# Kernel tuning notes

Measured on AMD Instinct MI355X. Metric: run time of the kernel, lower is better.

## Reference

```python
import jax, jax.numpy as jnp
import numpy as np
import math

N_HEAD = 16

def setup_inputs() -> dict:
    key = jax.random.key(0)
    k1, k2, k3 = jax.random.split(key, 3)
    B, S, D = 4, 2048, 1024
    hidden_states = jax.random.normal(k1, (B, S, D), dtype=jnp.float32)
    W_attn = jax.random.normal(k2, (D, 3 * D), dtype=jnp.float32) * 0.02
    b_attn = jnp.zeros((3 * D,), dtype=jnp.float32)
    W_proj = jax.random.normal(k3, (D, D), dtype=jnp.float32) * 0.02
    b_proj = jnp.zeros((D,), dtype=jnp.float32)
    return {"hidden_states": hidden_states, "W_attn": W_attn, "b_attn": b_attn,
            "W_proj": W_proj, "b_proj": b_proj}

def reference(hidden_states, W_attn, b_attn, W_proj, b_proj):
    B, S, D = hidden_states.shape
    H = N_HEAD
    hd = D // H
    # c_attn (GPT-2 Conv1D): x @ W + b -> [B, S, 3D]
    qkv = hidden_states @ W_attn + b_attn
    q, k, v = jnp.split(qkv, 3, axis=-1)
    # split heads -> [B, H, S, hd]
    def split_heads(t):
        return t.reshape(B, S, H, hd).transpose(0, 2, 1, 3)
    q, k, v = split_heads(q), split_heads(k), split_heads(v)
    # scores = QK^T / sqrt(hd)  -> [B, H, S, S]
    scores = jnp.einsum('bhqd,bhkd->bhqk', q, k) / math.sqrt(hd)
    # causal mask, multiplicative + additive as in source
    causal = jnp.tril(jnp.ones((S, S), dtype=scores.dtype))[None, None]
    scores = scores * causal + (-10000.0) * (1.0 - causal)
    attn_weights = jax.nn.softmax(scores, axis=-1)
    context = jnp.einsum('bhqk,bhkd->bhqd', attn_weights, v)
    # merge heads -> [B, S, D]
    attn_output = context.transpose(0, 2, 1, 3).reshape(B, S, D)
    # c_proj
    out = attn_output @ W_proj + b_proj
    return out
```

## Files before the change

### kernel.cpp

```cpp
#include <hip/hip_runtime.h>
#include <stdint.h>

typedef __attribute__((ext_vector_type(8))) short short8;
typedef __attribute__((ext_vector_type(8))) __bf16 bf16x8v;
typedef __attribute__((ext_vector_type(4))) float f32x4;

#define GLOBAL_AS __attribute__((address_space(1)))
#define LDS_AS __attribute__((address_space(3)))

__device__ __forceinline__ void gl2lds16(const void* g, void* l) {
  __builtin_amdgcn_global_load_lds((const GLOBAL_AS void*)g, (LDS_AS void*)l, 16, 0, 0);
}

__device__ __forceinline__ unsigned short f2bf(float x) {
  unsigned int u = __builtin_bit_cast(unsigned int, x);
  return (unsigned short)((u + 0x7fffu + ((u >> 16) & 1u)) >> 16);
}

__device__ __forceinline__ float bf2f(unsigned short u) {
  unsigned int v = (unsigned int)u << 16;
  return __builtin_bit_cast(float, v);
}

__device__ __forceinline__ unsigned cvtpk(float lo, float hi) {
  unsigned r;
  asm volatile("v_cvt_pk_bf16_f32 %0, %1, %2" : "=v"(r) : "v"(lo), "v"(hi));
  return r;
}

__device__ __forceinline__ short8 ldv8(const unsigned short* p) {
  return *(const short8*)p;
}

template <typename T>
__device__ __forceinline__ auto mfma_impl(T a, T b, f32x4 c, int)
    -> decltype(__builtin_amdgcn_mfma_f32_16x16x32_bf16(a, b, c, 0, 0, 0)) {
  return __builtin_amdgcn_mfma_f32_16x16x32_bf16(a, b, c, 0, 0, 0);
}
template <typename T>
__device__ __forceinline__ f32x4 mfma_impl(T a, T b, f32x4 c, long) {
  bf16x8v aa = __builtin_bit_cast(bf16x8v, a);
  bf16x8v bb = __builtin_bit_cast(bf16x8v, b);
  return __builtin_amdgcn_mfma_f32_16x16x32_bf16(aa, bb, c, 0, 0, 0);
}
__device__ __forceinline__ f32x4 mfma16(short8 a, short8 b, f32x4 c) {
  return mfma_impl(a, b, c, 0);
}

__global__ __launch_bounds__(256) void cast_bf16_kernel(const float* __restrict__ X,
                                                        unsigned short* __restrict__ Y,
                                                        int n4) {
  int i = blockIdx.x * 256 + threadIdx.x;
  if (i >= n4) return;
  const float4 v = ((const float4*)X)[i];
  unsigned long long pk = (unsigned long long)f2bf(v.x)
                        | ((unsigned long long)f2bf(v.y) << 16)
                        | ((unsigned long long)f2bf(v.z) << 32)
                        | ((unsigned long long)f2bf(v.w) << 48);
  ((unsigned long long*)Y)[i] = pk;
}

__global__ __launch_bounds__(256) void transpose_cast_kernel(const float* __restrict__ W,
                                                             unsigned short* __restrict__ Wt,
                                                             int Kd, int Nd) {
  __shared__ unsigned short tile[32][33];
  const int n0 = blockIdx.x * 32, k0 = blockIdx.y * 32;
  const int tx = threadIdx.x & 31, ty = threadIdx.x >> 5;
  #pragma unroll
  for (int i = 0; i < 4; ++i)
    tile[ty + i * 8][tx] = f2bf(W[(long)(k0 + ty + i * 8) * Nd + n0 + tx]);
  __syncthreads();
  #pragma unroll
  for (int i = 0; i < 4; ++i)
    Wt[(long)(n0 + ty + i * 8) * Kd + k0 + tx] = tile[tx][ty + i * 8];
}

template <int MODE>
__global__ __launch_bounds__(256) void gemm_kernel(
    const unsigned short* __restrict__ A,
    const unsigned short* __restrict__ Wt,
    const float* __restrict__ bias,
    float* __restrict__ Cout,
    unsigned short* __restrict__ Qb,
    unsigned short* __restrict__ Kb,
    unsigned short* __restrict__ Vt,
    int M, int N, int K) {
  __shared__ __align__(16) unsigned short Asm[2][128 * 32];
  __shared__ __align__(16) unsigned short Bsm[2][128 * 32];
  const int tid = threadIdx.x;
  const int w = tid >> 6, l = tid & 63;
  const int m0 = blockIdx.y * 128, n0 = blockIdx.x * 128;
  const int wr = (w >> 1) * 64, wc = (w & 1) * 64;
  const int laneRow = l & 15, laneG = l >> 4;

  const f32x4 z4 = {0.f, 0.f, 0.f, 0.f};
  f32x4 acc[4][4];
  #pragma unroll
  for (int m = 0; m < 4; ++m)
    #pragma unroll
    for (int n = 0; n < 4; ++n) acc[m][n] = z4;

  const int srow = tid >> 2;
  const int scol = (tid & 3) * 8;
  const unsigned short* Ag = A + (long)(m0 + srow) * K + scol;
  const unsigned short* Bg = Wt + (long)(n0 + srow) * K + scol;

  const int aoff = (wr + laneRow) * 32 + laneG * 8;
  const int boff = (wc + laneRow) * 32 + laneG * 8;

  auto STAGE = [&](int buf, int kt) {
    gl2lds16(Ag + kt, &Asm[buf][w * 512]);
    gl2lds16(Ag + (long)64 * K + kt, &Asm[buf][2048 + w * 512]);
    gl2lds16(Bg + kt, &Bsm[buf][w * 512]);
    gl2lds16(Bg + (long)64 * K + kt, &Bsm[buf][2048 + w * 512]);
  };

  int cur = 0;
  STAGE(0, 0);
  asm volatile("s_waitcnt vmcnt(0)" ::: "memory");
  __builtin_amdgcn_s_barrier();

  for (int kt = 0; kt < K; kt += 32) {
    if (kt + 32 < K) STAGE(cur ^ 1, kt + 32);
    short8 af[4], bfr[4];
    #pragma unroll
    for (int m = 0; m < 4; ++m) af[m] = ldv8(&Asm[cur][aoff + m * 512]);
    #pragma unroll
    for (int n = 0; n < 4; ++n) bfr[n] = ldv8(&Bsm[cur][boff + n * 512]);
    #pragma unroll
    for (int m = 0; m < 4; ++m)
      #pragma unroll
      for (int n = 0; n < 4; ++n)
        acc[m][n] = mfma16(af[m], bfr[n], acc[m][n]);
    asm volatile("s_waitcnt vmcnt(0)" ::: "memory");
    __builtin_amdgcn_s_barrier();
    cur ^= 1;
  }

  if (MODE == 0 && n0 >= 2048) {
    #pragma unroll
    for (int m = 0; m < 4; ++m) {
      const int row_base = m0 + wr + m * 16 + laneG * 4;
      #pragma unroll
      for (int n = 0; n < 4; ++n) {
        const int col = n0 + wc + n * 16 + laneRow;
        const float bv = bias[col];
        const int d = col & 1023;
        const int h = d >> 6, e = d & 63;
        const int bb = row_base >> 11, s = row_base & 2047;
        unsigned long long pk = (unsigned long long)f2bf(acc[m][n][0] + bv)
                              | ((unsigned long long)f2bf(acc[m][n][1] + bv) << 16)
                              | ((unsigned long long)f2bf(acc[m][n][2] + bv) << 32)
                              | ((unsigned long long)f2bf(acc[m][n][3] + bv) << 48);
        *(unsigned long long*)(Vt + ((long)((bb * 16 + h) * 64 + e)) * 2048 + s) = pk;
      }
    }
    return;
  }

  float* ep = ((w < 2) ? (float*)Asm : (float*)Bsm) + (w & 1) * 1088;
  const int c0 = (l & 7) * 8;
  const int rrow = l >> 3;
  const int colg0 = n0 + wc + c0;
  float bv[8];
  #pragma unroll
  for (int j = 0; j < 8; ++j) bv[j] = bias[colg0 + j];
  unsigned short* Tqk = (colg0 >> 10) ? Kb : Qb;
  const int hh = (colg0 & 1023) >> 6, e0 = colg0 & 63;

  #pragma unroll
  for (int m = 0; m < 4; ++m) {
    asm volatile("s_waitcnt lgkmcnt(0)" ::: "memory");
    #pragma unroll
    for (int n = 0; n < 4; ++n)
      #pragma unroll
      for (int r = 0; r < 4; ++r)
        ep[(laneG * 4 + r) * 68 + n * 16 + laneRow] = acc[m][n][r];
    asm volatile("s_waitcnt lgkmcnt(0)" ::: "memory");
    #pragma unroll
    for (int j = 0; j < 2; ++j) {
      const int row = rrow + j * 8;
      f32x4 va = *(const f32x4*)&ep[row * 68 + c0];
      f32x4 vb = *(const f32x4*)&ep[row * 68 + c0 + 4];
      va[0] += bv[0]; va[1] += bv[1]; va[2] += bv[2]; va[3] += bv[3];
      vb[0] += bv[4]; vb[1] += bv[5]; vb[2] += bv[6]; vb[3] += bv[7];
      const int row_g = m0 + wr + m * 16 + row;
      if (MODE == 1) {
        *(f32x4*)&Cout[(long)row_g * N + colg0] = va;
        *(f32x4*)&Cout[(long)row_g * N + colg0 + 4] = vb;
      } else {
        uint4 pk;
        pk.x = cvtpk(va[0], va[1]);
        pk.y = cvtpk(va[2], va[3]);
        pk.z = cvtpk(vb[0], vb[1]);
        pk.w = cvtpk(vb[2], vb[3]);
        const int bb = row_g >> 11, s = row_g & 2047;
        *(uint4*)(Tqk + ((long)(bb * 16 + hh) * 2048 + s) * 64 + e0) = pk;
      }
    }
  }
}

__global__ __launch_bounds__(512) void attn_kernel(
    const unsigned short* __restrict__ Qb,
    const unsigned short* __restrict__ Kb,
    const unsigned short* __restrict__ Vt,
    unsigned short* __restrict__ Ao) {
  __shared__ __align__(16) unsigned short Ksm[2][64 * 64];
  __shared__ __align__(16) unsigned short Vsm[2][64 * 64];
  __shared__ __align__(16) unsigned short Psm[8][16][72];

  const int tid = threadIdx.x;
  const int w = tid >> 6, l = tid & 63;
  const int bid = blockIdx.x;
  const int px = bid >> 6;
  const int y = ((bid & 7) << 3) | ((bid >> 3) & 7);
  const int laneRow = l & 15, g = l >> 4;
  const unsigned short* Qh = Qb + (long)y * (2048 * 64);
  const unsigned short* Kh = Kb + (long)y * (2048 * 64);
  const unsigned short* Vh = Vt + (long)y * (64 * 2048);

  const int srow = tid >> 3;
  const int sxor = ((tid & 7) ^ (srow & 7)) * 8;
  const int b = y >> 4, h = y & 15;
  const f32x4 z4 = {0.f, 0.f, 0.f, 0.f};
  short8 ones8;
  #pragma unroll
  for (int j = 0; j < 8; ++j) ones8[j] = (short)0x3F80;

  auto STAGE = [&](int buf, int kt) {
    gl2lds16(Kh + (long)kt * 4096 + srow * 64 + sxor, &Ksm[buf][w * 512]);
    gl2lds16(Vh + kt * 64 + (long)srow * 2048 + sxor, &Vsm[buf][w * 512]);
  };

  for (int pass = 0; pass < 2; ++pass) {
    const int x = pass ? (15 - px) : px;
    const int q0 = x * 128;
    const int qlo = w * 16;

    const float QS = 0.18033688011112042f;
    short8 qf[2];
    {
      short8 r0 = ldv8(Qh + (q0 + qlo + laneRow) * 64 + g * 8);
      short8 r1 = ldv8(Qh + (q0 + qlo + laneRow) * 64 + 32 + g * 8);
      #pragma unroll
      for (int j = 0; j < 8; ++j) {
        qf[0][j] = (short)f2bf(bf2f((unsigned short)r0[j]) * QS);
        qf[1][j] = (short)f2bf(bf2f((unsigned short)r1[j]) * QS);
      }
    }

    float lr[4] = {0.f, 0.f, 0.f, 0.f};
    f32x4 o[4];
    #pragma unroll
    for (int i = 0; i < 4; ++i) o[i] = z4;

    const int nkt = 2 * x + 2;
    int cur = 0;
    STAGE(0, 0);
    asm volatile("s_waitcnt vmcnt(0)" ::: "memory");
    __builtin_amdgcn_s_barrier();

    for (int kt = 0; kt < nkt; ++kt) {
      if (kt + 1 < nkt) STAGE(cur ^ 1, kt + 1);

      const int keybase = kt * 64 - q0;
      const bool fullskip = keybase > qlo + 15;

      if (!fullskip) {
        f32x4 sc[4];
        __builtin_amdgcn_s_setprio(1);
        #pragma unroll
        for (int n = 0; n < 4; ++n) {
          const int krow = n * 16 + laneRow;
          short8 b0 = ldv8(&Ksm[cur][krow * 64 + ((g ^ (krow & 7)) * 8)]);
          short8 b1 = ldv8(&Ksm[cur][krow * 64 + (((g + 4) ^ (krow & 7)) * 8)]);
          f32x4 a = mfma16(b0, qf[0], z4);
          sc[n] = mfma16(b1, qf[1], a);
        }
        __builtin_amdgcn_s_setprio(0);

        if (keybase + 63 > qlo) {
          #pragma unroll
          for (int n = 0; n < 4; ++n) {
            const int keyb = keybase + n * 16 + g * 4;
            #pragma unroll
            for (int r = 0; r < 4; ++r)
              if (keyb + r > qlo + laneRow) sc[n][r] = -1e9f;
          }
        }

        #pragma unroll
        for (int n = 0; n < 4; ++n)
          #pragma unroll
          for (int r = 0; r < 4; ++r)
            sc[n][r] = exp2f(sc[n][r]);

        #pragma unroll
        for (int n = 0; n < 4; ++n) {
          uint2 pk;
          pk.x = cvtpk(sc[n][0], sc[n][1]);
          pk.y = cvtpk(sc[n][2], sc[n][3]);
          *(uint2*)&Psm[w][laneRow][n * 16 + g * 4] = pk;
        }
        asm volatile("s_waitcnt lgkmcnt(0)" ::: "memory");

        f32x4 rs = z4;
        #pragma unroll
        for (int kk = 0; kk < 2; ++kk) {
          short8 pf = ldv8(&Psm[w][laneRow][kk * 32 + g * 8]);
          __builtin_amdgcn_s_setprio(1);
          #pragma unroll
          for (int n2 = 0; n2 < 4; ++n2) {
            const int vrow = n2 * 16 + laneRow;
            short8 vf = ldv8(&Vsm[cur][vrow * 64 + (((g + kk * 4) ^ (vrow & 7)) * 8)]);
            o[n2] = mfma16(pf, vf, o[n2]);
          }
          rs = mfma16(pf, ones8, rs);
          __builtin_amdgcn_s_setprio(0);
        }
        #pragma unroll
        for (int r = 0; r < 4; ++r) lr[r] += rs[r];
      }

      asm volatile("s_waitcnt vmcnt(0)" ::: "memory");
      __builtin_amdgcn_s_barrier();
      cur ^= 1;
    }

    #pragma unroll
    for (int n2 = 0; n2 < 4; ++n2) {
      #pragma unroll
      for (int r = 0; r < 4; ++r) {
        float v = o[n2][r] / lr[r];
        long row = (long)b * 2048 + q0 + qlo + g * 4 + r;
        Ao[row * 1024 + h * 64 + n2 * 16 + laneRow] = f2bf(v);
      }
    }
  }
}

extern "C" void kernel_launch(void* const* d_in, const int* in_sizes, int n_in,
                              void* d_out, int out_size, void* d_ws, size_t ws_size,
                              hipStream_t stream) {
  const float* hs = (const float*)d_in[0];
  const float* W_attn = (const float*)d_in[1];
  const float* b_attn = (const float*)d_in[2];
  const float* W_proj = (const float*)d_in[3];
  const float* b_proj = (const float*)d_in[4];
  float* out = (float*)d_out;

  const size_t SZ_HS = 16777216;
  const size_t SZ_WA = 6291456;
  const size_t SZ_WP = 2097152;
  const size_t SZ_T = 16777216;
  if (ws_size < SZ_HS + SZ_WA + SZ_WP + 4 * SZ_T) return;

  char* p = (char*)d_ws;
  unsigned short* hs_bf = (unsigned short*)p; p += SZ_HS;
  unsigned short* WtA = (unsigned short*)p;   p += SZ_WA;
  unsigned short* WtP = (unsigned short*)p;   p += SZ_WP;
  unsigned short* Qb = (unsigned short*)p;    p += SZ_T;
  unsigned short* Kb = (unsigned short*)p;    p += SZ_T;
  unsigned short* Vt = (unsigned short*)p;    p += SZ_T;
  unsigned short* Ao = (unsigned short*)p;    p += SZ_T;

  cast_bf16_kernel<<<8192, 256, 0, stream>>>(hs, hs_bf, 8192 * 1024 / 4);
  transpose_cast_kernel<<<dim3(96, 32), 256, 0, stream>>>(W_attn, WtA, 1024, 3072);
  transpose_cast_kernel<<<dim3(32, 32), 256, 0, stream>>>(W_proj, WtP, 1024, 1024);
  gemm_kernel<0><<<dim3(24, 64), 256, 0, stream>>>(hs_bf, WtA, b_attn, nullptr, Qb, Kb, Vt,
                                                   8192, 3072, 1024);
  attn_kernel<<<512, 512, 0, stream>>>(Qb, Kb, Vt, Ao);
  gemm_kernel<1><<<dim3(8, 64), 256, 0, stream>>>(Ao, WtP, b_proj, out, nullptr, nullptr, nullptr,
                                                  8192, 1024, 1024);
}
```

Baseline: 192.0 us.

## Replace QKV GEMM with 256x256-tile, 8-wave, swizzled-LDS pipelined kernel

The QKV projection now runs in a dedicated kernel with 256x256 output tiles, 512 threads and two LDS buffers of half-K sub-tiles. Loads go straight to LDS through global_load_lds with an XOR swizzle. Each iteration splits the MFMA work into four phases separated by barriers and s_setprio, so the next tile prefetches while the current one computes. The larger tile is meant to cut global and LDS traffic per FLOP and to hide load latency. In exchange it uses more registers and LDS, launches only 384 blocks (low occupancy), and adds barrier overhead. The output projection keeps the old kernel with the QKV-specific code removed.

```diff
diff --git a/kernel.cpp b/kernel.cpp
--- a/kernel.cpp
+++ b/kernel.cpp
@@ -75,15 +75,201 @@
     Wt[(long)(n0 + ty + i * 8) * Kd + k0 + tx] = tile[tx][ty + i * 8];
 }
 
-template <int MODE>
-__global__ __launch_bounds__(256) void gemm_kernel(
+__global__ __launch_bounds__(512, 2) void gemm256_qkv(
+    const unsigned short* __restrict__ A,
+    const unsigned short* __restrict__ Wt,
+    const float* __restrict__ bias,
+    unsigned short* __restrict__ Qb,
+    unsigned short* __restrict__ Kb,
+    unsigned short* __restrict__ Vt) {
+  constexpr int K = 1024, NK = 16;
+  __shared__ __align__(16) unsigned short Ab[2][2][8192];
+  __shared__ __align__(16) unsigned short Bb[2][2][8192];
+
+  const int tid = threadIdx.x;
+  const int w = tid >> 6, l = tid & 63;
+  const int n0 = blockIdx.x * 256, m0 = blockIdx.y * 256;
+  const int wr = (w >> 2) * 128;
+  const int wc = (w & 3) * 64;
+  const int lr16 = l & 15, g2 = l >> 4;
+
+  const unsigned short* Ag = A + (long)m0 * K;
+  const unsigned short* Bg = Wt + (long)n0 * K;
+
+  auto STG = [&](unsigned short* Lh, const unsigned short* Gb) {
+    #pragma unroll
+    for (int i = 0; i < 2; ++i) {
+      const int s = i * 512 + tid;
+      const int r = s >> 2;
+      const int gsl = (s & 3) ^ (r & 3);
+      gl2lds16(Gb + (long)r * K + gsl * 8, Lh + (i * 512 + w * 64) * 8);
+    }
+  };
+
+  const f32x4 z4 = {0.f, 0.f, 0.f, 0.f};
+  f32x4 acc[8][4];
+  #pragma unroll
+  for (int m = 0; m < 8; ++m)
+    #pragma unroll
+    for (int n = 0; n < 4; ++n) acc[m][n] = z4;
+
+  STG(&Bb[0][0][0], Bg + 0);
+  STG(&Ab[0][0][0], Ag + 0);
+  STG(&Bb[0][1][0], Bg + 32);
+  STG(&Ab[0][1][0], Ag + 32);
+  STG(&Bb[1][0][0], Bg + 64);
+  STG(&Ab[1][0][0], Ag + 64);
+  STG(&Bb[1][1][0], Bg + 96);
+  asm volatile("s_waitcnt vmcnt(6)" ::: "memory");
+  asm volatile("s_barrier" ::: "memory");
+
+  short8 af[4], bf[4];
+  for (int t = 0; t < NK; ++t) {
+    const int c = t & 1;
+    #pragma unroll
+    for (int ni = 0; ni < 4; ++ni) {
+      const int row = wc + ni * 16 + lr16;
+      bf[ni] = ldv8(&Bb[c][0][row * 32 + ((g2 ^ (row & 3)) * 8)]);
+    }
+    #pragma unroll
+    for (int mi = 0; mi < 4; ++mi) {
+      const int row = wr + mi * 16 + lr16;
+      af[mi] = ldv8(&Ab[c][0][row * 32 + ((g2 ^ (row & 3)) * 8)]);
+    }
+    if (t + 1 < NK) STG(&Ab[c ^ 1][1][0], Ag + (t + 1) * 64 + 32);
+    asm volatile("s_barrier" ::: "memory");
+    __builtin_amdgcn_s_setprio(1);
+    #pragma unroll
+    for (int mi = 0; mi < 4; ++mi)
+      #pragma unroll
+      for (int ni = 0; ni < 4; ++ni)
+        acc[mi][ni] = mfma16(af[mi], bf[ni], acc[mi][ni]);
+    __builtin_amdgcn_s_setprio(0);
+    asm volatile("s_barrier" ::: "memory");
+
+    #pragma unroll
+    for (int mi = 0; mi < 4; ++mi) {
+      const int row = wr + 64 + mi * 16 + lr16;
+      af[mi] = ldv8(&Ab[c][0][row * 32 + ((g2 ^ (row & 3)) * 8)]);
+    }
+    if (t + 2 < NK) STG(&Bb[c][0][0], Bg + (t + 2) * 64);
+    asm volatile("s_barrier" ::: "memory");
+    __builtin_amdgcn_s_setprio(1);
+    #pragma unroll
+    for (int mi = 0; mi < 4; ++mi)
+      #pragma unroll
+      for (int ni = 0; ni < 4; ++ni)
+        acc[4 + mi][ni] = mfma16(af[mi], bf[ni], acc[4 + mi][ni]);
+    __builtin_amdgcn_s_setprio(0);
+    asm volatile("s_barrier" ::: "memory");
+
+    #pragma unroll
+    for (int ni = 0; ni < 4; ++ni) {
+      const int row = wc + ni * 16 + lr16;
+      bf[ni] = ldv8(&Bb[c][1][row * 32 + ((g2 ^ (row & 3)) * 8)]);
+    }
+    #pragma unroll
+    for (int mi = 0; mi < 4; ++mi) {
+      const int row = wr + mi * 16 + lr16;
+      af[mi] = ldv8(&Ab[c][1][row * 32 + ((g2 ^ (row & 3)) * 8)]);
+    }
+    if (t + 2 < NK) STG(&Ab[c][0][0], Ag + (t + 2) * 64);
+    asm volatile("s_barrier" ::: "memory");
+    __builtin_amdgcn_s_setprio(1);
+    #pragma unroll
+    for (int mi = 0; mi < 4; ++mi)
+      #pragma unroll
+      for (int ni = 0; ni < 4; ++ni)
+        acc[mi][ni] = mfma16(af[mi], bf[ni], acc[mi][ni]);
+    __builtin_amdgcn_s_setprio(0);
+    asm volatile("s_barrier" ::: "memory");
+
+    #pragma unroll
+    for (int mi = 0; mi < 4; ++mi) {
+      const int row = wr + 64 + mi * 16 + lr16;
+      af[mi] = ldv8(&Ab[c][1][row * 32 + ((g2 ^ (row & 3)) * 8)]);
+    }
+    if (t + 2 < NK) STG(&Bb[c][1][0], Bg + (t + 2) * 64 + 32);
+    asm volatile("s_barrier" ::: "memory");
+    __builtin_amdgcn_s_setprio(1);
+    #pragma unroll
+    for (int mi = 0; mi < 4; ++mi)
+      #pragma unroll
+      for (int ni = 0; ni < 4; ++ni)
+        acc[4 + mi][ni] = mfma16(af[mi], bf[ni], acc[4 + mi][ni]);
+    __builtin_amdgcn_s_setprio(0);
+    if (t + 2 >= NK) {
+      asm volatile("s_waitcnt vmcnt(0)" ::: "memory");
+    } else {
+      asm volatile("s_waitcnt vmcnt(6)" ::: "memory");
+    }
+    asm volatile("s_barrier" ::: "memory");
+  }
+
+  if (n0 >= 2048) {
+    #pragma unroll
+    for (int mi = 0; mi < 8; ++mi) {
+      const int row_base = m0 + wr + mi * 16 + g2 * 4;
+      #pragma unroll
+      for (int ni = 0; ni < 4; ++ni) {
+        const int col = n0 + wc + ni * 16 + lr16;
+        const float bv = bias[col];
+        const int d = col & 1023;
+        const int h = d >> 6, e = d & 63;
+        const int bb = row_base >> 11, s = row_base & 2047;
+        unsigned long long pk = (unsigned long long)f2bf(acc[mi][ni][0] + bv)
+                              | ((unsigned long long)f2bf(acc[mi][ni][1] + bv) << 16)
+                              | ((unsigned long long)f2bf(acc[mi][ni][2] + bv) << 32)
+                              | ((unsigned long long)f2bf(acc[mi][ni][3] + bv) << 48);
+        *(unsigned long long*)(Vt + ((long)((bb * 16 + h) * 64 + e)) * 2048 + s) = pk;
+      }
+    }
+    return;
+  }
+
+  float* ep = (float*)&Ab[0][0][0] + w * 1088;
+  const int c0 = (l & 7) * 8;
+  const int rrow = l >> 3;
+  const int colg0 = n0 + wc + c0;
+  float bv[8];
+  #pragma unroll
+  for (int j = 0; j < 8; ++j) bv[j] = bias[colg0 + j];
+  unsigned short* Tqk = ((n0 + wc) >> 10) ? Kb : Qb;
+  const int hh = ((n0 + wc) & 1023) >> 6;
+
+  #pragma unroll
+  for (int mi = 0; mi < 8; ++mi) {
+    asm volatile("s_waitcnt lgkmcnt(0)" ::: "memory");
+    #pragma unroll
+    for (int ni = 0; ni < 4; ++ni)
+      #pragma unroll
+      for (int r = 0; r < 4; ++r)
+        ep[(g2 * 4 + r) * 68 + ni * 16 + lr16] = acc[mi][ni][r];
+    asm volatile("s_waitcnt lgkmcnt(0)" ::: "memory");
+    #pragma unroll
+    for (int j = 0; j < 2; ++j) {
+      const int row = rrow + j * 8;
+      f32x4 va = *(const f32x4*)&ep[row * 68 + c0];
+      f32x4 vb = *(const f32x4*)&ep[row * 68 + c0 + 4];
+      va[0] += bv[0]; va[1] += bv[1]; va[2] += bv[2]; va[3] += bv[3];
+      vb[0] += bv[4]; vb[1] += bv[5]; vb[2] += bv[6]; vb[3] += bv[7];
+      const int row_g = m0 + wr + mi * 16 + row;
+      uint4 pk;
+      pk.x = cvtpk(va[0], va[1]);
+      pk.y = cvtpk(va[2], va[3]);
+      pk.z = cvtpk(vb[0], vb[1]);
+      pk.w = cvtpk(vb[2], vb[3]);
+      const int bb = row_g >> 11, s = row_g & 2047;
+      *(uint4*)(Tqk + ((long)(bb * 16 + hh) * 2048 + s) * 64 + c0) = pk;
+    }
+  }
+}
+
+__global__ __launch_bounds__(256) void gemm_proj(
     const unsigned short* __restrict__ A,
     const unsigned short* __restrict__ Wt,
     const float* __restrict__ bias,
     float* __restrict__ Cout,
-    unsigned short* __restrict__ Qb,
-    unsigned short* __restrict__ Kb,
-    unsigned short* __restrict__ Vt,
     int M, int N, int K) {
   __shared__ __align__(16) unsigned short Asm[2][128 * 32];
   __shared__ __align__(16) unsigned short Bsm[2][128 * 32];
@@ -137,27 +323,6 @@
     cur ^= 1;
   }
 
-  if (MODE == 0 && n0 >= 2048) {
-    #pragma unroll
-    for (int m = 0; m < 4; ++m) {
-      const int row_base = m0 + wr + m * 16 + laneG * 4;
-      #pragma unroll
-      for (int n = 0; n < 4; ++n) {
-        const int col = n0 + wc + n * 16 + laneRow;
-        const float bv = bias[col];
-        const int d = col & 1023;
-        const int h = d >> 6, e = d & 63;
-        const int bb = row_base >> 11, s = row_base & 2047;
-        unsigned long long pk = (unsigned long long)f2bf(acc[m][n][0] + bv)
-                              | ((unsigned long long)f2bf(acc[m][n][1] + bv) << 16)
-                              | ((unsigned long long)f2bf(acc[m][n][2] + bv) << 32)
-                              | ((unsigned long long)f2bf(acc[m][n][3] + bv) << 48);
-        *(unsigned long long*)(Vt + ((long)((bb * 16 + h) * 64 + e)) * 2048 + s) = pk;
-      }
-    }
-    return;
-  }
-
   float* ep = ((w < 2) ? (float*)Asm : (float*)Bsm) + (w & 1) * 1088;
   const int c0 = (l & 7) * 8;
   const int rrow = l >> 3;
@@ -165,8 +330,6 @@
   float bv[8];
   #pragma unroll
   for (int j = 0; j < 8; ++j) bv[j] = bias[colg0 + j];
-  unsigned short* Tqk = (colg0 >> 10) ? Kb : Qb;
-  const int hh = (colg0 & 1023) >> 6, e0 = colg0 & 63;
 
   #pragma unroll
   for (int m = 0; m < 4; ++m) {
@@ -185,18 +348,8 @@
       va[0] += bv[0]; va[1] += bv[1]; va[2] += bv[2]; va[3] += bv[3];
       vb[0] += bv[4]; vb[1] += bv[5]; vb[2] += bv[6]; vb[3] += bv[7];
       const int row_g = m0 + wr + m * 16 + row;
-      if (MODE == 1) {
-        *(f32x4*)&Cout[(long)row_g * N + colg0] = va;
-        *(f32x4*)&Cout[(long)row_g * N + colg0 + 4] = vb;
-      } else {
-        uint4 pk;
-        pk.x = cvtpk(va[0], va[1]);
-        pk.y = cvtpk(va[2], va[3]);
-        pk.z = cvtpk(vb[0], vb[1]);
-        pk.w = cvtpk(vb[2], vb[3]);
-        const int bb = row_g >> 11, s = row_g & 2047;
-        *(uint4*)(Tqk + ((long)(bb * 16 + hh) * 2048 + s) * 64 + e0) = pk;
-      }
+      *(f32x4*)&Cout[(long)row_g * N + colg0] = va;
+      *(f32x4*)&Cout[(long)row_g * N + colg0 + 4] = vb;
     }
   }
 }
@@ -368,9 +521,7 @@
   cast_bf16_kernel<<<8192, 256, 0, stream>>>(hs, hs_bf, 8192 * 1024 / 4);
   transpose_cast_kernel<<<dim3(96, 32), 256, 0, stream>>>(W_attn, WtA, 1024, 3072);
   transpose_cast_kernel<<<dim3(32, 32), 256, 0, stream>>>(W_proj, WtP, 1024, 1024);
-  gemm_kernel<0><<<dim3(24, 64), 256, 0, stream>>>(hs_bf, WtA, b_attn, nullptr, Qb, Kb, Vt,
-                                                   8192, 3072, 1024);
+  gemm256_qkv<<<dim3(12, 32), 512, 0, stream>>>(hs_bf, WtA, b_attn, Qb, Kb, Vt);
   attn_kernel<<<512, 512, 0, stream>>>(Qb, Kb, Vt, Ao);
-  gemm_kernel<1><<<dim3(8, 64), 256, 0, stream>>>(Ao, WtP, b_proj, out, nullptr, nullptr, nullptr,
-                                                  8192, 1024, 1024);
-}
+  gemm_proj<<<dim3(8, 64), 256, 0, stream>>>(Ao, WtP, b_proj, out, 8192, 1024, 1024);
+}
```

Result: slower. 200.5 us (+4.4%).

## Triple-buffer GEMM LDS pipeline and remap blocks for XCD-aware L2 locality

Applied to the files above, without the earlier changes.

The GEMM kernel moves from double to triple buffering of the A/B LDS tiles. Loads run two k-steps ahead and a partial vmcnt wait keeps one stage in flight. Raising wave priority around the MFMA block and setting launch bounds to 3 blocks/CU are meant to improve overlap. A 1D grid is remapped so consecutive blocks on the same XCD share A rows and B columns for better L2 reuse, at the cost of more LDS per block, which could limit occupancy.

```diff
diff --git a/kernel.cpp b/kernel.cpp
--- a/kernel.cpp
+++ b/kernel.cpp
@@ -76,7 +76,7 @@
 }
 
 template <int MODE>
-__global__ __launch_bounds__(256) void gemm_kernel(
+__global__ __launch_bounds__(256, 3) void gemm_kernel(
     const unsigned short* __restrict__ A,
     const unsigned short* __restrict__ Wt,
     const float* __restrict__ bias,
@@ -85,11 +85,23 @@
     unsigned short* __restrict__ Kb,
     unsigned short* __restrict__ Vt,
     int M, int N, int K) {
-  __shared__ __align__(16) unsigned short Asm[2][128 * 32];
-  __shared__ __align__(16) unsigned short Bsm[2][128 * 32];
+  __shared__ __align__(16) unsigned short Asm[3][128 * 32];
+  __shared__ __align__(16) unsigned short Bsm[3][128 * 32];
   const int tid = threadIdx.x;
   const int w = tid >> 6, l = tid & 63;
-  const int m0 = blockIdx.y * 128, n0 = blockIdx.x * 128;
+
+  const int bid = blockIdx.x;
+  const int xcd = bid & 7, tt = bid >> 3;
+  int xb, yb;
+  if (MODE == 0) {
+    xb = (xcd & 1) * 12 + tt % 12;
+    yb = (xcd >> 1) * 16 + tt / 12;
+  } else {
+    xb = tt & 7;
+    yb = xcd * 8 + (tt >> 3);
+  }
+  const int m0 = yb * 128, n0 = xb * 128;
+
   const int wr = (w >> 1) * 64, wc = (w & 1) * 64;
   const int laneRow = l & 15, laneG = l >> 4;
 
@@ -115,26 +127,35 @@
     gl2lds16(Bg + (long)64 * K + kt, &Bsm[buf][2048 + w * 512]);
   };
 
-  int cur = 0;
+  const int NT = K >> 5;
   STAGE(0, 0);
-  asm volatile("s_waitcnt vmcnt(0)" ::: "memory");
-  __builtin_amdgcn_s_barrier();
-
-  for (int kt = 0; kt < K; kt += 32) {
-    if (kt + 32 < K) STAGE(cur ^ 1, kt + 32);
+  STAGE(1, 32);
+  asm volatile("s_waitcnt vmcnt(4)" ::: "memory");
+  asm volatile("s_barrier" ::: "memory");
+
+  int cur = 0, sb = 2;
+  for (int t = 0; t < NT; ++t) {
+    if (t + 2 < NT) STAGE(sb, (t + 2) * 32);
     short8 af[4], bfr[4];
     #pragma unroll
     for (int m = 0; m < 4; ++m) af[m] = ldv8(&Asm[cur][aoff + m * 512]);
     #pragma unroll
     for (int n = 0; n < 4; ++n) bfr[n] = ldv8(&Bsm[cur][boff + n * 512]);
+    __builtin_amdgcn_s_setprio(1);
     #pragma unroll
     for (int m = 0; m < 4; ++m)
       #pragma unroll
       for (int n = 0; n < 4; ++n)
         acc[m][n] = mfma16(af[m], bfr[n], acc[m][n]);
-    asm volatile("s_waitcnt vmcnt(0)" ::: "memory");
-    __builtin_amdgcn_s_barrier();
-    cur ^= 1;
+    __builtin_amdgcn_s_setprio(0);
+    if (t + 2 < NT) {
+      asm volatile("s_waitcnt vmcnt(4)" ::: "memory");
+    } else {
+      asm volatile("s_waitcnt vmcnt(0)" ::: "memory");
+    }
+    asm volatile("s_barrier" ::: "memory");
+    cur = (cur == 2) ? 0 : cur + 1;
+    sb = (sb == 2) ? 0 : sb + 1;
   }
 
   if (MODE == 0 && n0 >= 2048) {
@@ -158,7 +179,7 @@
     return;
   }
 
-  float* ep = ((w < 2) ? (float*)Asm : (float*)Bsm) + (w & 1) * 1088;
+  float* ep = (float*)&Asm[0][0] + w * 1088;
   const int c0 = (l & 7) * 8;
   const int rrow = l >> 3;
   const int colg0 = n0 + wc + c0;
@@ -368,9 +389,9 @@
   cast_bf16_kernel<<<8192, 256, 0, stream>>>(hs, hs_bf, 8192 * 1024 / 4);
   transpose_cast_kernel<<<dim3(96, 32), 256, 0, stream>>>(W_attn, WtA, 1024, 3072);
   transpose_cast_kernel<<<dim3(32, 32), 256, 0, stream>>>(W_proj, WtP, 1024, 1024);
-  gemm_kernel<0><<<dim3(24, 64), 256, 0, stream>>>(hs_bf, WtA, b_attn, nullptr, Qb, Kb, Vt,
-                                                   8192, 3072, 1024);
+  gemm_kernel<0><<<1536, 256, 0, stream>>>(hs_bf, WtA, b_attn, nullptr, Qb, Kb, Vt,
+                                           8192, 3072, 1024);
   attn_kernel<<<512, 512, 0, stream>>>(Qb, Kb, Vt, Ao);
-  gemm_kernel<1><<<dim3(8, 64), 256, 0, stream>>>(Ao, WtP, b_proj, out, nullptr, nullptr, nullptr,
-                                                  8192, 1024, 1024);
-}
+  gemm_kernel<1><<<512, 256, 0, stream>>>(Ao, WtP, b_proj, out, nullptr, nullptr, nullptr,
+                                          8192, 1024, 1024);
+}
```

Result: faster. 181.4 us (-5.5%).
